# Kernel tuning notes

Hardware: AMD Instinct MI355X
Metric: run time of the kernel (lower is better)

## Reference

```python
import jax, jax.numpy as jnp
import numpy as np

B, L, LH, D, H = 32, 512, 2048, 1024, 4
DK = D // H  # dot-attn head dim
NEG = -1e9


def _ln(x, g, b, eps=1e-5):
    m = x.mean(-1, keepdims=True)
    v = ((x - m) ** 2).mean(-1, keepdims=True)
    return (x - m) / jnp.sqrt(v + eps) * g + b


def setup_inputs() -> dict:
    key = jax.random.key(0)
    ks = jax.random.split(key, 16)
    s = 0.05
    inp = {
        "seq_emb": jax.random.normal(ks[0], (B, L, D), jnp.float32),
        "seq_mask": jnp.ones((B, L), jnp.float32),
        "his_seq_emb": jax.random.normal(ks[1], (B, LH, D), jnp.float32),
        "his_seq_mask": jnp.ones((B, LH), jnp.float32),
        # dot-product MHA (bias=True)
        "sa_wq": jax.random.normal(ks[2], (D, D), jnp.float32) * s,
        "sa_bq": jnp.zeros((D,), jnp.float32),
        "sa_wk": jax.random.normal(ks[3], (D, D), jnp.float32) * s,
        "sa_bk": jnp.zeros((D,), jnp.float32),
        "sa_wv": jax.random.normal(ks[4], (D, D), jnp.float32) * s,
        "sa_bv": jnp.zeros((D,), jnp.float32),
        "sa_wo": jax.random.normal(ks[5], (D, D), jnp.float32) * s,
        "sa_bo": jnp.zeros((D,), jnp.float32),
        # short LayerNorm
        "sn_g": jnp.ones((D,), jnp.float32),
        "sn_b": jnp.zeros((D,), jnp.float32),
        # additive MHA (h=1, bias=False)
        "aa_wq": jax.random.normal(ks[6], (D, D), jnp.float32) * s,
        "aa_wk": jax.random.normal(ks[7], (D, D), jnp.float32) * s,
        "aa_wv": jax.random.normal(ks[8], (D, D), jnp.float32) * s,
        "aa_wo": jax.random.normal(ks[9], (D, D), jnp.float32) * s,
        "aa_wa": jax.random.normal(ks[10], (D,), jnp.float32) * s,
        # long LayerNorm
        "ln_g": jnp.ones((D,), jnp.float32),
        "ln_b": jnp.zeros((D,), jnp.float32),
    }
    return inp


def reference(seq_emb, seq_mask, his_seq_emb, his_seq_mask,
              sa_wq, sa_bq, sa_wk, sa_bk, sa_wv, sa_bv, sa_wo, sa_bo,
              sn_g, sn_b, aa_wq, aa_wk, aa_wv, aa_wo, aa_wa, ln_g, ln_b):
    # ---- dot-product self attention over seq_emb (dropout = eval/no-op) ----
    def split_heads(x):  # (B,L,D) -> (B,H,L,DK)
        return x.reshape(B, -1, H, DK).transpose(0, 2, 1, 3)

    q = split_heads(seq_emb @ sa_wq + sa_bq)
    k = split_heads(seq_emb @ sa_wk + sa_bk)
    v = split_heads(seq_emb @ sa_wv + sa_bv)
    scores = jnp.einsum('bhqd,bhkd->bhqk', q, k) / jnp.sqrt(jnp.float32(DK))
    scores = jnp.where(seq_mask[:, None, None, :] == 0, NEG, scores)
    p_attn = jax.nn.softmax(scores, axis=-1)  # (B,H,L,L)
    ctx = jnp.einsum('bhqk,bhkd->bhqd', p_attn, v)
    ctx = ctx.transpose(0, 2, 1, 3).reshape(B, L, D)
    sa_out = ctx @ sa_wo + sa_bo

    poi_attn = _ln(sa_out, sn_g, sn_b) * seq_mask[:, :, None]
    poi_hidden = poi_attn.mean(axis=1, keepdims=True)  # (B,1,D)

    # ---- additive (Bahdanau) attention, h=1, Lq=1 ----
    aq = poi_hidden @ aa_wq        # (B,1,D)
    ak = his_seq_emb @ aa_wk       # (B,LH,D)
    av = his_seq_emb @ aa_wv       # (B,LH,D)
    feats = jnp.tanh(aq[:, :, None, :] + ak[:, None, :, :])  # (B,1,LH,D)
    a_scores = jnp.einsum('bqkd,d->bqk', feats, aa_wa)        # (B,1,LH)
    a_scores = jnp.where(his_seq_mask[:, None, :] == 0, NEG, a_scores)
    a_w = jax.nn.softmax(a_scores, axis=-1)
    a_ctx = jnp.einsum('bqk,bkd->bqd', a_w, av)               # (B,1,D)
    aa_out = a_ctx @ aa_wo

    his_poi_hidden = poi_hidden + _ln(aa_out, ln_g, ln_b)     # (B,1,D)

    attn_weight = p_attn[:, 0, :, :]                          # (B,L,L)
    seq_hidden = jnp.concatenate([poi_hidden, his_poi_hidden], axis=-1)[:, 0, :]  # (B,2D)
    return seq_hidden, attn_weight
```

## Files before the change

kernel.cpp:

```cpp
#include <hip/hip_runtime.h>

#define NEGV (-1000000000.0f)

typedef __attribute__((ext_vector_type(8))) short sh8;
typedef __attribute__((ext_vector_type(4))) short sh4;
typedef __attribute__((ext_vector_type(8))) __bf16 bf16x8;
typedef __attribute__((ext_vector_type(4))) float f32x4;

__device__ __forceinline__ float b2f(unsigned short u) {
  unsigned v = ((unsigned)u) << 16;
  return __builtin_bit_cast(float, v);
}
__device__ __forceinline__ unsigned short f2b(float f) {
  unsigned x = __builtin_bit_cast(unsigned, f);
  unsigned r = (x + 0x7fffu + ((x >> 16) & 1u)) >> 16;
  return (unsigned short)r;
}
__device__ __forceinline__ void g2l16(const void* g, void* l) {
  __builtin_amdgcn_global_load_lds((const __attribute__((address_space(1))) unsigned int*)g,
                                   (__attribute__((address_space(3))) unsigned int*)l, 16, 0, 0);
}
__device__ __forceinline__ f32x4 mfma16(bf16x8 a, bf16x8 b, f32x4 c) {
  return __builtin_amdgcn_mfma_f32_16x16x32_bf16(a, b, c, 0, 0, 0);
}
__device__ __forceinline__ float fast_tanh(float x) {
  x = fminf(fmaxf(x, -15.f), 15.f);
  float e = __expf(2.f * x);
  return (e - 1.f) / (e + 1.f);
}

__global__ void cvt_all(const float* __restrict__ sa, unsigned short* __restrict__ da, int n4a,
                        const float* __restrict__ sb, unsigned short* __restrict__ db, int n4b)
{
  int stride = gridDim.x * blockDim.x;
  int i0 = blockIdx.x * blockDim.x + threadIdx.x;
  for (int i = i0; i < n4a; i += stride) {
    float4 v = ((const float4*)sa)[i];
    sh4 o;
    o[0] = (short)f2b(v.x); o[1] = (short)f2b(v.y);
    o[2] = (short)f2b(v.z); o[3] = (short)f2b(v.w);
    ((sh4*)da)[i] = o;
  }
  for (int i = i0; i < n4b; i += stride) {
    float4 v = ((const float4*)sb)[i];
    sh4 o;
    o[0] = (short)f2b(v.x); o[1] = (short)f2b(v.y);
    o[2] = (short)f2b(v.z); o[3] = (short)f2b(v.w);
    ((sh4*)db)[i] = o;
  }
}

__global__ void tcvt5(const float* __restrict__ s0, const float* __restrict__ s1,
                      const float* __restrict__ s2, const float* __restrict__ s3,
                      const float* __restrict__ s4,
                      unsigned short* __restrict__ d0, unsigned short* __restrict__ d1,
                      unsigned short* __restrict__ d2, unsigned short* __restrict__ d3,
                      unsigned short* __restrict__ d4)
{
  __shared__ float tile[64][65];
  const float* src; unsigned short* dst;
  switch (blockIdx.z) {
    case 0: src = s0; dst = d0; break;
    case 1: src = s1; dst = d1; break;
    case 2: src = s2; dst = d2; break;
    case 3: src = s3; dst = d3; break;
    default: src = s4; dst = d4; break;
  }
  int bx = blockIdx.x, by = blockIdx.y;
  int tx = threadIdx.x & 63, ty = threadIdx.x >> 6;
#pragma unroll
  for (int i = 0; i < 16; ++i) {
    int r = i * 4 + ty;
    tile[r][tx] = src[(size_t)(by * 64 + r) * 1024 + bx * 64 + tx];
  }
  __syncthreads();
#pragma unroll
  for (int i = 0; i < 16; ++i) {
    int r = i * 4 + ty;
    dst[(size_t)(bx * 64 + r) * 1024 + by * 64 + tx] = f2b(tile[tx][r]);
  }
}

template<int EPI>
__global__ __launch_bounds__(512, 1)
void gemm256(const unsigned short* __restrict__ A, const unsigned short* __restrict__ Bt,
             int nbx, int nby, int bxm,
             const float* __restrict__ b0, const float* __restrict__ b1,
             const float* __restrict__ b2,
             unsigned short* __restrict__ O0, unsigned short* __restrict__ O1,
             unsigned short* __restrict__ O2,
             const float* __restrict__ aq, const float* __restrict__ wa,
             float* __restrict__ sc)
{
  __shared__ char lds[131072];
  const int tid = threadIdx.x;
  const int w = tid >> 6, l = tid & 63;
  const int wm = w >> 2, wn = w & 3;
  const int lr = l & 15, g = l >> 4;

  const int wg = blockIdx.x;
  const int cpx = gridDim.x >> 3;
  const int wgid = (wg & 7) * cpx + (wg >> 3);
  int bx, by;
  if (bxm) { bx = wgid / nby; by = wgid - bx * nby; }
  else     { bx = wgid % nbx; by = wgid / nbx; }
  const size_t m0 = (size_t)by * 256;
  const int n0 = bx * 256;

  f32x4 acc[8][4] = {};
  bf16x8 fa[4], fb[4];

  const int srow = w * 8 + (l >> 3);
  const int schunk = ((l & 7) ^ ((l >> 3) & 7)) * 8;
  const unsigned short* gA = A + (m0 + srow) * 1024 + schunk;
  const unsigned short* gB = Bt + ((size_t)n0 + srow) * 1024 + schunk;
  const int ldst = w * 1024;

  const int chs = lr & 7;
  const int aRd0 = wm * 16384 + lr * 128;
  const int bRd0 = 32768 + (wn >> 1) * 16384 + (wn & 1) * 8192 + lr * 128;
  const int ck0 = ((0 * 4 + g) ^ chs) * 16;
  const int ck1 = ((1 * 4 + g) ^ chs) * 16;

#define STG_A(BUF, AH, RH, KK) \
  g2l16(gA + ((AH) * 128 + (RH) * 64) * 1024 + (KK), \
        lds + (BUF) * 65536 + (AH) * 16384 + (RH) * 8192 + ldst)
#define STG_B(BUF, BH, RH, KK) \
  g2l16(gB + ((BH) * 128 + (RH) * 64) * 1024 + (KK), \
        lds + (BUF) * 65536 + 32768 + (BH) * 16384 + (RH) * 8192 + ldst)

#define PH(BUFOFF, CK, IH, STAGES, TAIL)                                      \
  {                                                                           \
    const char* pb_ = lds + (BUFOFF);                                         \
    if ((IH) == 0) {                                                          \
      _Pragma("unroll") for (int j = 0; j < 4; ++j)                           \
        fb[j] = *(const bf16x8*)(pb_ + bRd0 + j * 2048 + (CK));               \
    }                                                                         \
    _Pragma("unroll") for (int i = 0; i < 4; ++i)                             \
      fa[i] = *(const bf16x8*)(pb_ + aRd0 + (IH) * 8192 + i * 2048 + (CK));   \
    STAGES;                                                                   \
    __builtin_amdgcn_sched_barrier(0);                                        \
    asm volatile("s_barrier" ::: "memory");                                   \
    asm volatile("s_waitcnt lgkmcnt(0)" ::: "memory");                        \
    __builtin_amdgcn_sched_barrier(0);                                        \
    __builtin_amdgcn_s_setprio(1);                                            \
    _Pragma("unroll") for (int i = 0; i < 4; ++i)                             \
      _Pragma("unroll") for (int j = 0; j < 4; ++j)                           \
        acc[(IH) * 4 + i][j] = mfma16(fa[i], fb[j], acc[(IH) * 4 + i][j]);    \
    __builtin_amdgcn_s_setprio(0);                                            \
    TAIL;                                                                     \
    asm volatile("s_barrier" ::: "memory");                                   \
  }

  STG_A(0, 0, 0, 0); STG_A(0, 0, 1, 0); STG_A(0, 1, 0, 0); STG_A(0, 1, 1, 0);
  STG_B(0, 0, 0, 0); STG_B(0, 0, 1, 0); STG_B(0, 1, 0, 0); STG_B(0, 1, 1, 0);
  STG_A(1, 0, 0, 64); STG_A(1, 1, 0, 64);
  asm volatile("s_waitcnt vmcnt(0)" ::: "memory");
  asm volatile("s_barrier" ::: "memory");

#pragma unroll 1
  for (int t = 0; t < 8; ++t) {
    const int k1 = (2 * t + 1) * 64, k2 = (2 * t + 2) * 64, k3 = (2 * t + 3) * 64;
    const bool st = (t < 7);
    PH(0,     ck0, 0, { STG_A(1, 0, 1, k1); STG_A(1, 1, 1, k1); }, {})
    PH(0,     ck0, 1, { STG_B(1, 0, 0, k1); STG_B(1, 0, 1, k1); }, {})
    PH(0,     ck1, 0, { STG_B(1, 1, 0, k1); STG_B(1, 1, 1, k1); }, {})
    PH(0,     ck1, 1, { if (st) { STG_A(0, 0, 0, k2); STG_A(0, 1, 0, k2); } },
       { if (st) { asm volatile("s_waitcnt vmcnt(2)" ::: "memory"); }
         else    { asm volatile("s_waitcnt vmcnt(0)" ::: "memory"); } })
    PH(65536, ck0, 0, { if (st) { STG_A(0, 0, 1, k2); STG_A(0, 1, 1, k2); } }, {})
    PH(65536, ck0, 1, { if (st) { STG_B(0, 0, 0, k2); STG_B(0, 0, 1, k2); } }, {})
    PH(65536, ck1, 0, { if (st) { STG_B(0, 1, 0, k2); STG_B(0, 1, 1, k2); } }, {})
    PH(65536, ck1, 1, { if (st) { STG_A(1, 0, 0, k3); STG_A(1, 1, 0, k3); } },
       { if (st) { asm volatile("s_waitcnt vmcnt(2)" ::: "memory"); } })
  }
#undef PH
#undef STG_A
#undef STG_B

  if (EPI == 0) {
#pragma unroll
    for (int j = 0; j < 4; ++j) {
      int col = n0 + wn * 64 + j * 16 + lr;
      float bv = b0[col];
#pragma unroll
      for (int i = 0; i < 8; ++i) {
        size_t rowb = m0 + wm * 128 + i * 16 + g * 4;
#pragma unroll
        for (int r = 0; r < 4; ++r)
          O0[(rowb + r) * 1024 + col] = f2b(acc[i][j][r] + bv);
      }
    }
  } else if (EPI == 1) {
#pragma unroll
    for (int j = 0; j < 4; ++j) {
      int col3 = n0 + wn * 64 + j * 16 + lr;
      int part = col3 >> 10, c = col3 & 1023;
      float bv = (part == 0) ? b0[c] : (part == 1) ? b1[c] : b2[c];
      if (part < 2) {
        unsigned short* O = part == 0 ? O0 : O1;
#pragma unroll
        for (int i = 0; i < 8; ++i) {
          size_t rowb = m0 + wm * 128 + i * 16 + g * 4;
#pragma unroll
          for (int r = 0; r < 4; ++r)
            O[(rowb + r) * 1024 + c] = f2b(acc[i][j][r] + bv);
        }
      } else {
        int h = c >> 8, d = c & 255;
#pragma unroll
        for (int i = 0; i < 8; ++i) {
          size_t row = m0 + wm * 128 + i * 16 + g * 4;
          int bb = (int)(row >> 9), ll = (int)(row & 511);
          size_t base = ((size_t)(bb * 4 + h) * 256 + d) * 512 + ll;
#pragma unroll
          for (int r = 0; r < 4; ++r)
            O2[base + r] = f2b(acc[i][j][r] + bv);
        }
      }
    }
  } else {
    const int bb = (int)(m0 >> 11);
#pragma unroll
    for (int i = 0; i < 8; ++i) {
      float rp[4] = {0.f, 0.f, 0.f, 0.f};
#pragma unroll
      for (int j = 0; j < 4; ++j) {
        int col = n0 + wn * 64 + j * 16 + lr;
        float wav = wa[col];
        float aqv = aq[bb * 1024 + col];
#pragma unroll
        for (int r = 0; r < 4; ++r)
          rp[r] += wav * fast_tanh(acc[i][j][r] + aqv);
      }
#pragma unroll
      for (int off = 1; off < 16; off <<= 1)
#pragma unroll
        for (int r = 0; r < 4; ++r)
          rp[r] += __shfl_xor(rp[r], off, 64);
      if (lr == 0) {
        size_t rowb = m0 + wm * 128 + i * 16 + g * 4;
#pragma unroll
        for (int r = 0; r < 4; ++r)
          atomicAdd(&sc[rowb + r], rp[r]);
      }
    }
  }
}

__global__ __launch_bounds__(256, 4)
void attn_kernel(const unsigned short* __restrict__ q, const unsigned short* __restrict__ k,
                 const unsigned short* __restrict__ vT, const float* __restrict__ seq_mask,
                 unsigned short* __restrict__ ctx, float* __restrict__ attn_out)
{
  __shared__ char smem[34304];
  unsigned short* Qs = (unsigned short*)smem;
  unsigned short* Ps = (unsigned short*)smem;
  float* redm = (float*)(smem + 33280);
  float* reds = (float*)(smem + 33792);
  const int t = threadIdx.x, w = t >> 6, l = t & 63;
  const int lr = l & 15, g = l >> 4, lk8 = g * 8;
  const int wg = blockIdx.x;
  const int wgid = (wg & 7) * 256 + (wg >> 3);
  const int qt = wgid & 15, bh = wgid >> 4;
  const int h = bh & 3, b = bh >> 2;
  const int l0 = qt * 32;

  for (int idx = t; idx < 32 * 32; idx += 256) {
    int r = idx >> 5, ch = (idx & 31) * 8;
    *(sh8*)&Qs[r * 264 + ch] =
        *(const sh8*)&q[((size_t)(b * 512 + l0 + r)) * 1024 + h * 256 + ch];
  }
  __syncthreads();

  f32x4 accs[2][8] = {};
  const unsigned short* kbase = k + ((size_t)b * 512) * 1024 + h * 256;
#pragma unroll
  for (int ds = 0; ds < 8; ++ds) {
    int d0 = ds * 32;
    bf16x8 a0 = *(const bf16x8*)&Qs[lr * 264 + d0 + lk8];
    bf16x8 a1 = *(const bf16x8*)&Qs[(16 + lr) * 264 + d0 + lk8];
#pragma unroll
    for (int j = 0; j < 8; ++j) {
      int kj = w * 128 + j * 16 + lr;
      bf16x8 bb = *(const bf16x8*)&kbase[(size_t)kj * 1024 + d0 + lk8];
      accs[0][j] = mfma16(a0, bb, accs[0][j]);
      accs[1][j] = mfma16(a1, bb, accs[1][j]);
    }
  }

#pragma unroll
  for (int j = 0; j < 8; ++j) {
    int col = w * 128 + j * 16 + lr;
    float mv = seq_mask[b * 512 + col];
    bool msk = (mv == 0.f);
#pragma unroll
    for (int i = 0; i < 2; ++i)
#pragma unroll
      for (int r = 0; r < 4; ++r)
        accs[i][j][r] = msk ? NEGV : accs[i][j][r] * 0.0625f;
  }

  float mx[2][4], sm[2][4];
#pragma unroll
  for (int i = 0; i < 2; ++i)
#pragma unroll
    for (int r = 0; r < 4; ++r) {
      float m = accs[i][0][r];
#pragma unroll
      for (int j = 1; j < 8; ++j) m = fmaxf(m, accs[i][j][r]);
      mx[i][r] = m;
    }
#pragma unroll
  for (int off = 1; off < 16; off <<= 1)
#pragma unroll
    for (int i = 0; i < 2; ++i)
#pragma unroll
      for (int r = 0; r < 4; ++r)
        mx[i][r] = fmaxf(mx[i][r], __shfl_xor(mx[i][r], off, 64));
  if (lr == 0) {
#pragma unroll
    for (int i = 0; i < 2; ++i)
#pragma unroll
      for (int r = 0; r < 4; ++r)
        redm[w * 32 + i * 16 + g * 4 + r] = mx[i][r];
  }
  __syncthreads();
#pragma unroll
  for (int i = 0; i < 2; ++i)
#pragma unroll
    for (int r = 0; r < 4; ++r) {
      int row = i * 16 + g * 4 + r;
      mx[i][r] = fmaxf(fmaxf(redm[row], redm[32 + row]),
                       fmaxf(redm[64 + row], redm[96 + row]));
      sm[i][r] = 0.f;
    }

#pragma unroll
  for (int i = 0; i < 2; ++i)
#pragma unroll
    for (int j = 0; j < 8; ++j)
#pragma unroll
      for (int r = 0; r < 4; ++r) {
        float p = __expf(accs[i][j][r] - mx[i][r]);
        accs[i][j][r] = p;
        sm[i][r] += p;
      }
#pragma unroll
  for (int off = 1; off < 16; off <<= 1)
#pragma unroll
    for (int i = 0; i < 2; ++i)
#pragma unroll
      for (int r = 0; r < 4; ++r)
        sm[i][r] += __shfl_xor(sm[i][r], off, 64);
  if (lr == 0) {
#pragma unroll
    for (int i = 0; i < 2; ++i)
#pragma unroll
      for (int r = 0; r < 4; ++r)
        reds[w * 32 + i * 16 + g * 4 + r] = sm[i][r];
  }
  __syncthreads();
#pragma unroll
  for (int i = 0; i < 2; ++i)
#pragma unroll
    for (int r = 0; r < 4; ++r) {
      int row = i * 16 + g * 4 + r;
      float s = reds[row] + reds[32 + row] + reds[64 + row] + reds[96 + row];
      sm[i][r] = 1.f / s;
    }

#pragma unroll
  for (int i = 0; i < 2; ++i)
#pragma unroll
    for (int j = 0; j < 8; ++j) {
      int col = w * 128 + j * 16 + lr;
#pragma unroll
      for (int r = 0; r < 4; ++r) {
        int row = i * 16 + g * 4 + r;
        float pn = accs[i][j][r] * sm[i][r];
        Ps[row * 520 + col] = f2b(pn);
        if (h == 0)
          attn_out[((size_t)(b * 512 + l0 + row)) * 512 + col] = pn;
      }
    }
  __syncthreads();

  f32x4 acco[2][4] = {};
  const unsigned short* vbase = vT + ((size_t)(b * 4 + h)) * 256 * 512;
#pragma unroll
  for (int ks = 0; ks < 16; ++ks) {
    int kj0 = ks * 32;
    bf16x8 a0 = *(const bf16x8*)&Ps[lr * 520 + kj0 + lk8];
    bf16x8 a1 = *(const bf16x8*)&Ps[(16 + lr) * 520 + kj0 + lk8];
#pragma unroll
    for (int j = 0; j < 4; ++j) {
      int d = w * 64 + j * 16 + lr;
      bf16x8 bb = *(const bf16x8*)&vbase[(size_t)d * 512 + kj0 + lk8];
      acco[0][j] = mfma16(a0, bb, acco[0][j]);
      acco[1][j] = mfma16(a1, bb, acco[1][j]);
    }
  }
#pragma unroll
  for (int i = 0; i < 2; ++i)
#pragma unroll
    for (int j = 0; j < 4; ++j) {
      int col = w * 64 + j * 16 + lr;
#pragma unroll
      for (int r = 0; r < 4; ++r) {
        int row = i * 16 + g * 4 + r;
        ctx[((size_t)(b * 512 + l0 + row)) * 1024 + h * 256 + col] = f2b(acco[i][j][r]);
      }
    }
}

__global__ __launch_bounds__(256)
void ln_mean(const unsigned short* __restrict__ sa, const float* __restrict__ g,
             const float* __restrict__ bt, const float* __restrict__ mask,
             float* __restrict__ poi_sum)
{
  const int b = blockIdx.y, ch = blockIdx.x;
  const int t = threadIdx.x, w = t >> 6, l = t & 63;
  float gg[16], bb[16];
#pragma unroll
  for (int j = 0; j < 16; ++j) { gg[j] = g[l * 16 + j]; bb[j] = bt[l * 16 + j]; }
  float accv[16];
#pragma unroll
  for (int j = 0; j < 16; ++j) accv[j] = 0.f;
  for (int rr = 0; rr < 16; ++rr) {
    int row = ch * 64 + w * 16 + rr;
    const unsigned short* rp = sa + ((size_t)(b * 512 + row)) * 1024 + l * 16;
    float x[16];
    sh8 v0 = *(const sh8*)rp;
    sh8 v1 = *(const sh8*)(rp + 8);
#pragma unroll
    for (int j = 0; j < 8; ++j) {
      x[j] = b2f((unsigned short)v0[j]);
      x[8 + j] = b2f((unsigned short)v1[j]);
    }
    float s = 0.f, s2 = 0.f;
#pragma unroll
    for (int j = 0; j < 16; ++j) { s += x[j]; s2 += x[j] * x[j]; }
#pragma unroll
    for (int off = 1; off < 64; off <<= 1) {
      s += __shfl_xor(s, off, 64);
      s2 += __shfl_xor(s2, off, 64);
    }
    float mean = s * (1.f / 1024.f);
    float var = s2 * (1.f / 1024.f) - mean * mean;
    float rinv = rsqrtf(var + 1e-5f);
    float mk = mask[b * 512 + row];
#pragma unroll
    for (int j = 0; j < 16; ++j) accv[j] += ((x[j] - mean) * rinv * gg[j] + bb[j]) * mk;
  }
#pragma unroll
  for (int j = 0; j < 16; ++j) atomicAdd(&poi_sum[b * 1024 + l * 16 + j], accv[j]);
}

__global__ void finalize_poi(const float* __restrict__ ps, float* __restrict__ poi) {
  int i = blockIdx.x * 256 + threadIdx.x;
  if (i < 32 * 1024) poi[i] = ps[i] * (1.f / 512.f);
}

__global__ __launch_bounds__(256)
void gemv32(const float* __restrict__ in, const float* __restrict__ W, float* __restrict__ out)
{
  const int b = blockIdx.y;
  const int n = blockIdx.x * 256 + threadIdx.x;
  const float* ib = in + b * 1024;
  float acc = 0.f;
  for (int d = 0; d < 1024; d += 4) {
    acc += ib[d]     * W[(size_t)d * 1024 + n]
         + ib[d + 1] * W[(size_t)(d + 1) * 1024 + n]
         + ib[d + 2] * W[(size_t)(d + 2) * 1024 + n]
         + ib[d + 3] * W[(size_t)(d + 3) * 1024 + n];
  }
  out[b * 1024 + n] = acc;
}

__global__ __launch_bounds__(256)
void softmax_his(float* __restrict__ sc, const float* __restrict__ mask)
{
  __shared__ float red[4];
  const int b = blockIdx.x, t = threadIdx.x, w = t >> 6, l = t & 63;
  float v[8];
  float mx = -3.0e38f;
#pragma unroll
  for (int i = 0; i < 8; ++i) {
    int kk = t + i * 256;
    float s = (mask[b * 2048 + kk] == 0.f) ? NEGV : sc[b * 2048 + kk];
    v[i] = s;
    mx = fmaxf(mx, s);
  }
#pragma unroll
  for (int off = 1; off < 64; off <<= 1) mx = fmaxf(mx, __shfl_xor(mx, off, 64));
  if (l == 0) red[w] = mx;
  __syncthreads();
  mx = fmaxf(fmaxf(red[0], red[1]), fmaxf(red[2], red[3]));
  float sum = 0.f;
#pragma unroll
  for (int i = 0; i < 8; ++i) { v[i] = __expf(v[i] - mx); sum += v[i]; }
#pragma unroll
  for (int off = 1; off < 64; off <<= 1) sum += __shfl_xor(sum, off, 64);
  __syncthreads();
  if (l == 0) red[w] = sum;
  __syncthreads();
  sum = red[0] + red[1] + red[2] + red[3];
  float inv = 1.f / sum;
#pragma unroll
  for (int i = 0; i < 8; ++i) sc[b * 2048 + t + i * 256] = v[i] * inv;
}

__global__ __launch_bounds__(256)
void hw_kernel(const float* __restrict__ aw, const unsigned short* __restrict__ his,
               float* __restrict__ hw)
{
  const int b = blockIdx.y, kc = blockIdx.x, t = threadIdx.x;
  const int cb = t * 4;
  float a0 = 0.f, a1 = 0.f, a2 = 0.f, a3 = 0.f;
  for (int kk = 0; kk < 256; ++kk) {
    int k = kc * 256 + kk;
    float wg = aw[b * 2048 + k];
    sh4 vv = *(const sh4*)&his[((size_t)(b * 2048 + k)) * 1024 + cb];
    a0 += wg * b2f((unsigned short)vv[0]);
    a1 += wg * b2f((unsigned short)vv[1]);
    a2 += wg * b2f((unsigned short)vv[2]);
    a3 += wg * b2f((unsigned short)vv[3]);
  }
  atomicAdd(&hw[b * 1024 + cb + 0], a0);
  atomicAdd(&hw[b * 1024 + cb + 1], a1);
  atomicAdd(&hw[b * 1024 + cb + 2], a2);
  atomicAdd(&hw[b * 1024 + cb + 3], a3);
}

__global__ __launch_bounds__(256)
void final_kernel(const float* __restrict__ aa_out, const float* __restrict__ g,
                  const float* __restrict__ bt, const float* __restrict__ poi,
                  float* __restrict__ out)
{
  __shared__ float r1[4], r2[4];
  const int b = blockIdx.x, t = threadIdx.x, w = t >> 6, l = t & 63;
  float x[4];
#pragma unroll
  for (int j = 0; j < 4; ++j) x[j] = aa_out[b * 1024 + t * 4 + j];
  float s = 0.f, s2 = 0.f;
#pragma unroll
  for (int j = 0; j < 4; ++j) { s += x[j]; s2 += x[j] * x[j]; }
#pragma unroll
  for (int off = 1; off < 64; off <<= 1) {
    s += __shfl_xor(s, off, 64);
    s2 += __shfl_xor(s2, off, 64);
  }
  if (l == 0) { r1[w] = s; r2[w] = s2; }
  __syncthreads();
  s = r1[0] + r1[1] + r1[2] + r1[3];
  s2 = r2[0] + r2[1] + r2[2] + r2[3];
  float mean = s * (1.f / 1024.f);
  float var = s2 * (1.f / 1024.f) - mean * mean;
  float rinv = rsqrtf(var + 1e-5f);
#pragma unroll
  for (int j = 0; j < 4; ++j) {
    int c = t * 4 + j;
    float lnv = (x[j] - mean) * rinv * g[c] + bt[c];
    float pv = poi[b * 1024 + c];
    out[b * 2048 + c] = pv;
    out[b * 2048 + 1024 + c] = pv + lnv;
  }
}

extern "C" void kernel_launch(void* const* d_in, const int* in_sizes, int n_in,
                              void* d_out, int out_size, void* d_ws, size_t ws_size,
                              hipStream_t stream)
{
  const float* seq_emb  = (const float*)d_in[0];
  const float* seq_mask = (const float*)d_in[1];
  const float* his_emb  = (const float*)d_in[2];
  const float* his_mask = (const float*)d_in[3];
  const float* sa_wq = (const float*)d_in[4];
  const float* sa_bq = (const float*)d_in[5];
  const float* sa_wk = (const float*)d_in[6];
  const float* sa_bk = (const float*)d_in[7];
  const float* sa_wv = (const float*)d_in[8];
  const float* sa_bv = (const float*)d_in[9];
  const float* sa_wo = (const float*)d_in[10];
  const float* sa_bo = (const float*)d_in[11];
  const float* sn_g  = (const float*)d_in[12];
  const float* sn_b  = (const float*)d_in[13];
  const float* aa_wq = (const float*)d_in[14];
  const float* aa_wk = (const float*)d_in[15];
  const float* aa_wv = (const float*)d_in[16];
  const float* aa_wo = (const float*)d_in[17];
  const float* aa_wa = (const float*)d_in[18];
  const float* ln_g  = (const float*)d_in[19];
  const float* ln_b  = (const float*)d_in[20];
  float* out = (float*)d_out;

  char* p = (char*)d_ws;
  size_t off = 0;
  auto alloc = [&](size_t bytes) -> void* {
    void* r = p + off;
    off += (bytes + 255) & ~(size_t)255;
    return r;
  };
  unsigned short* seqb = (unsigned short*)alloc((size_t)16384 * 1024 * 2);
  unsigned short* hisb = (unsigned short*)alloc((size_t)65536 * 1024 * 2);
  unsigned short* wcat = (unsigned short*)alloc((size_t)3072 * 1024 * 2);
  unsigned short* woT  = (unsigned short*)alloc((size_t)1024 * 1024 * 2);
  unsigned short* awkT = (unsigned short*)alloc((size_t)1024 * 1024 * 2);
  unsigned short* qb   = (unsigned short*)alloc((size_t)16384 * 1024 * 2);
  unsigned short* kb   = (unsigned short*)alloc((size_t)16384 * 1024 * 2);
  unsigned short* vTb  = (unsigned short*)alloc((size_t)16384 * 1024 * 2);
  unsigned short* ctxb = (unsigned short*)alloc((size_t)16384 * 1024 * 2);
  unsigned short* saob = (unsigned short*)alloc((size_t)16384 * 1024 * 2);
  float* poi_sum = (float*)alloc((size_t)32 * 1024 * 4);
  float* poi     = (float*)alloc((size_t)32 * 1024 * 4);
  float* aqb     = (float*)alloc((size_t)32 * 1024 * 4);
  float* ascore  = (float*)alloc((size_t)32 * 2048 * 4);
  float* hwb     = (float*)alloc((size_t)32 * 1024 * 4);
  float* actx    = (float*)alloc((size_t)32 * 1024 * 4);
  float* aaout   = (float*)alloc((size_t)32 * 1024 * 4);
  if (off > ws_size) return;

  hipMemsetAsync(poi_sum, 0, (size_t)32 * 1024 * 4, stream);
  hipMemsetAsync(ascore, 0, (size_t)32 * 2048 * 4, stream);
  hipMemsetAsync(hwb, 0, (size_t)32 * 1024 * 4, stream);

  cvt_all<<<2048, 256, 0, stream>>>(seq_emb, seqb, 16384 * 1024 / 4,
                                    his_emb, hisb, 65536 * 1024 / 4);
  tcvt5<<<dim3(16, 16, 5), 256, 0, stream>>>(
      sa_wq, sa_wk, sa_wv, sa_wo, aa_wk,
      wcat, wcat + (size_t)1024 * 1024, wcat + (size_t)2048 * 1024, woT, awkT);

  gemm256<1><<<768, 512, 0, stream>>>(seqb, wcat, 12, 64, 1, sa_bq, sa_bk, sa_bv,
                                      qb, kb, vTb, nullptr, nullptr, nullptr);

  attn_kernel<<<2048, 256, 0, stream>>>(qb, kb, vTb, seq_mask, ctxb, out + 65536);

  gemm256<0><<<256, 512, 0, stream>>>(ctxb, woT, 4, 64, 0, sa_bo, nullptr, nullptr,
                                      saob, nullptr, nullptr, nullptr, nullptr, nullptr);
  ln_mean<<<dim3(8, 32), 256, 0, stream>>>(saob, sn_g, sn_b, seq_mask, poi_sum);
  finalize_poi<<<128, 256, 0, stream>>>(poi_sum, poi);
  gemv32<<<dim3(4, 32), 256, 0, stream>>>(poi, aa_wq, aqb);

  gemm256<2><<<1024, 512, 0, stream>>>(hisb, awkT, 4, 256, 0, nullptr, nullptr, nullptr,
                                       nullptr, nullptr, nullptr, aqb, aa_wa, ascore);
  softmax_his<<<32, 256, 0, stream>>>(ascore, his_mask);
  hw_kernel<<<dim3(8, 32), 256, 0, stream>>>(ascore, hisb, hwb);
  gemv32<<<dim3(4, 32), 256, 0, stream>>>(hwb, aa_wv, actx);
  gemv32<<<dim3(4, 32), 256, 0, stream>>>(actx, aa_wo, aaout);
  final_kernel<<<32, 256, 0, stream>>>(aaout, ln_g, ln_b, poi, out);
}
```

Measured before the change: 788.4 us.

## Replace 256x256 pipelined GEMM with simple 128x128 tile kernel and fuse poi finalize into gemv

Replaces the hand-pipelined 256x256-tile, 512-thread GEMM that uses 128KB of double-buffered LDS with a 128x128-tile, 256-thread kernel. The new kernel has a 32-wide K step, a single small LDS buffer, two __syncthreads per step and no prefetch overlap, and it launches more blocks with up to four per CU. The poi finalize kernel is also merged into the aa_wq gemv, which scales by 1/512 after the dot product, saving one launch. The simpler GEMM gives up the global-load/MFMA overlap and halves data reuse per tile, so it risks exposing memory latency.

```diff
diff --git a/kernel.cpp b/kernel.cpp
--- a/kernel.cpp
+++ b/kernel.cpp
@@ -82,9 +82,9 @@
 }
 
 template<int EPI>
-__global__ __launch_bounds__(512, 1)
-void gemm256(const unsigned short* __restrict__ A, const unsigned short* __restrict__ Bt,
-             int nbx, int nby, int bxm,
+__global__ __launch_bounds__(256, 4)
+void gemm128(const unsigned short* __restrict__ A, const unsigned short* __restrict__ Bt,
+             int nbx,
              const float* __restrict__ b0, const float* __restrict__ b1,
              const float* __restrict__ b2,
              unsigned short* __restrict__ O0, unsigned short* __restrict__ O1,
@@ -92,100 +92,66 @@
              const float* __restrict__ aq, const float* __restrict__ wa,
              float* __restrict__ sc)
 {
-  __shared__ char lds[131072];
+  __shared__ unsigned short ldsA[4096];
+  __shared__ unsigned short ldsB[4096];
   const int tid = threadIdx.x;
   const int w = tid >> 6, l = tid & 63;
-  const int wm = w >> 2, wn = w & 3;
+  const int wr = w >> 1, wc = w & 1;
   const int lr = l & 15, g = l >> 4;
 
   const int wg = blockIdx.x;
   const int cpx = gridDim.x >> 3;
   const int wgid = (wg & 7) * cpx + (wg >> 3);
-  int bx, by;
-  if (bxm) { bx = wgid / nby; by = wgid - bx * nby; }
-  else     { bx = wgid % nbx; by = wgid / nbx; }
-  const size_t m0 = (size_t)by * 256;
-  const int n0 = bx * 256;
-
-  f32x4 acc[8][4] = {};
-  bf16x8 fa[4], fb[4];
-
-  const int srow = w * 8 + (l >> 3);
-  const int schunk = ((l & 7) ^ ((l >> 3) & 7)) * 8;
-  const unsigned short* gA = A + (m0 + srow) * 1024 + schunk;
-  const unsigned short* gB = Bt + ((size_t)n0 + srow) * 1024 + schunk;
-  const int ldst = w * 1024;
-
-  const int chs = lr & 7;
-  const int aRd0 = wm * 16384 + lr * 128;
-  const int bRd0 = 32768 + (wn >> 1) * 16384 + (wn & 1) * 8192 + lr * 128;
-  const int ck0 = ((0 * 4 + g) ^ chs) * 16;
-  const int ck1 = ((1 * 4 + g) ^ chs) * 16;
-
-#define STG_A(BUF, AH, RH, KK) \
-  g2l16(gA + ((AH) * 128 + (RH) * 64) * 1024 + (KK), \
-        lds + (BUF) * 65536 + (AH) * 16384 + (RH) * 8192 + ldst)
-#define STG_B(BUF, BH, RH, KK) \
-  g2l16(gB + ((BH) * 128 + (RH) * 64) * 1024 + (KK), \
-        lds + (BUF) * 65536 + 32768 + (BH) * 16384 + (RH) * 8192 + ldst)
-
-#define PH(BUFOFF, CK, IH, STAGES, TAIL)                                      \
-  {                                                                           \
-    const char* pb_ = lds + (BUFOFF);                                         \
-    if ((IH) == 0) {                                                          \
-      _Pragma("unroll") for (int j = 0; j < 4; ++j)                           \
-        fb[j] = *(const bf16x8*)(pb_ + bRd0 + j * 2048 + (CK));               \
-    }                                                                         \
-    _Pragma("unroll") for (int i = 0; i < 4; ++i)                             \
-      fa[i] = *(const bf16x8*)(pb_ + aRd0 + (IH) * 8192 + i * 2048 + (CK));   \
-    STAGES;                                                                   \
-    __builtin_amdgcn_sched_barrier(0);                                        \
-    asm volatile("s_barrier" ::: "memory");                                   \
-    asm volatile("s_waitcnt lgkmcnt(0)" ::: "memory");                        \
-    __builtin_amdgcn_sched_barrier(0);                                        \
-    __builtin_amdgcn_s_setprio(1);                                            \
-    _Pragma("unroll") for (int i = 0; i < 4; ++i)                             \
-      _Pragma("unroll") for (int j = 0; j < 4; ++j)                           \
-        acc[(IH) * 4 + i][j] = mfma16(fa[i], fb[j], acc[(IH) * 4 + i][j]);    \
-    __builtin_amdgcn_s_setprio(0);                                            \
-    TAIL;                                                                     \
-    asm volatile("s_barrier" ::: "memory");                                   \
-  }
-
-  STG_A(0, 0, 0, 0); STG_A(0, 0, 1, 0); STG_A(0, 1, 0, 0); STG_A(0, 1, 1, 0);
-  STG_B(0, 0, 0, 0); STG_B(0, 0, 1, 0); STG_B(0, 1, 0, 0); STG_B(0, 1, 1, 0);
-  STG_A(1, 0, 0, 64); STG_A(1, 1, 0, 64);
-  asm volatile("s_waitcnt vmcnt(0)" ::: "memory");
-  asm volatile("s_barrier" ::: "memory");
+  const int bx = wgid % nbx, by = wgid / nbx;
+  const size_t m0 = (size_t)by * 128;
+  const int n0 = bx * 128;
+
+  f32x4 acc[4][4] = {};
+
+  const int srow = tid >> 2;
+  const int sk = ((tid & 3) ^ ((tid >> 2) & 3)) * 8;
+  const unsigned short* gA = A + (m0 + srow) * 1024 + sk;
+  const unsigned short* gB = Bt + ((size_t)n0 + srow) * 1024 + sk;
+  char* const dA0 = (char*)ldsA + w * 1024;
+  char* const dA1 = (char*)ldsA + 4096 + w * 1024;
+  char* const dB0 = (char*)ldsB + w * 1024;
+  char* const dB1 = (char*)ldsB + 4096 + w * 1024;
+
+  const int cswz = (g ^ (lr & 3)) * 16;
+  const int aoff = (wr * 64 + lr) * 64 + cswz;
+  const int boff = (wc * 64 + lr) * 64 + cswz;
 
 #pragma unroll 1
-  for (int t = 0; t < 8; ++t) {
-    const int k1 = (2 * t + 1) * 64, k2 = (2 * t + 2) * 64, k3 = (2 * t + 3) * 64;
-    const bool st = (t < 7);
-    PH(0,     ck0, 0, { STG_A(1, 0, 1, k1); STG_A(1, 1, 1, k1); }, {})
-    PH(0,     ck0, 1, { STG_B(1, 0, 0, k1); STG_B(1, 0, 1, k1); }, {})
-    PH(0,     ck1, 0, { STG_B(1, 1, 0, k1); STG_B(1, 1, 1, k1); }, {})
-    PH(0,     ck1, 1, { if (st) { STG_A(0, 0, 0, k2); STG_A(0, 1, 0, k2); } },
-       { if (st) { asm volatile("s_waitcnt vmcnt(2)" ::: "memory"); }
-         else    { asm volatile("s_waitcnt vmcnt(0)" ::: "memory"); } })
-    PH(65536, ck0, 0, { if (st) { STG_A(0, 0, 1, k2); STG_A(0, 1, 1, k2); } }, {})
-    PH(65536, ck0, 1, { if (st) { STG_B(0, 0, 0, k2); STG_B(0, 0, 1, k2); } }, {})
-    PH(65536, ck1, 0, { if (st) { STG_B(0, 1, 0, k2); STG_B(0, 1, 1, k2); } }, {})
-    PH(65536, ck1, 1, { if (st) { STG_A(1, 0, 0, k3); STG_A(1, 1, 0, k3); } },
-       { if (st) { asm volatile("s_waitcnt vmcnt(2)" ::: "memory"); } })
-  }
-#undef PH
-#undef STG_A
-#undef STG_B
+  for (int kt = 0; kt < 32; ++kt) {
+    const int k0 = kt * 32;
+    g2l16(gA + k0, dA0);
+    g2l16(gA + 64 * 1024 + k0, dA1);
+    g2l16(gB + k0, dB0);
+    g2l16(gB + 64 * 1024 + k0, dB1);
+    __syncthreads();
+    bf16x8 af[4], bf[4];
+#pragma unroll
+    for (int i = 0; i < 4; ++i)
+      af[i] = *(const bf16x8*)((const char*)ldsA + aoff + i * 1024);
+#pragma unroll
+    for (int j = 0; j < 4; ++j)
+      bf[j] = *(const bf16x8*)((const char*)ldsB + boff + j * 1024);
+#pragma unroll
+    for (int i = 0; i < 4; ++i)
+#pragma unroll
+      for (int j = 0; j < 4; ++j)
+        acc[i][j] = mfma16(af[i], bf[j], acc[i][j]);
+    __syncthreads();
+  }
 
   if (EPI == 0) {
 #pragma unroll
     for (int j = 0; j < 4; ++j) {
-      int col = n0 + wn * 64 + j * 16 + lr;
+      int col = n0 + wc * 64 + j * 16 + lr;
       float bv = b0[col];
 #pragma unroll
-      for (int i = 0; i < 8; ++i) {
-        size_t rowb = m0 + wm * 128 + i * 16 + g * 4;
+      for (int i = 0; i < 4; ++i) {
+        size_t rowb = m0 + wr * 64 + i * 16 + g * 4;
 #pragma unroll
         for (int r = 0; r < 4; ++r)
           O0[(rowb + r) * 1024 + col] = f2b(acc[i][j][r] + bv);
@@ -194,14 +160,14 @@
   } else if (EPI == 1) {
 #pragma unroll
     for (int j = 0; j < 4; ++j) {
-      int col3 = n0 + wn * 64 + j * 16 + lr;
+      int col3 = n0 + wc * 64 + j * 16 + lr;
       int part = col3 >> 10, c = col3 & 1023;
       float bv = (part == 0) ? b0[c] : (part == 1) ? b1[c] : b2[c];
       if (part < 2) {
         unsigned short* O = part == 0 ? O0 : O1;
 #pragma unroll
-        for (int i = 0; i < 8; ++i) {
-          size_t rowb = m0 + wm * 128 + i * 16 + g * 4;
+        for (int i = 0; i < 4; ++i) {
+          size_t rowb = m0 + wr * 64 + i * 16 + g * 4;
 #pragma unroll
           for (int r = 0; r < 4; ++r)
             O[(rowb + r) * 1024 + c] = f2b(acc[i][j][r] + bv);
@@ -209,8 +175,8 @@
       } else {
         int h = c >> 8, d = c & 255;
 #pragma unroll
-        for (int i = 0; i < 8; ++i) {
-          size_t row = m0 + wm * 128 + i * 16 + g * 4;
+        for (int i = 0; i < 4; ++i) {
+          size_t row = m0 + wr * 64 + i * 16 + g * 4;
           int bb = (int)(row >> 9), ll = (int)(row & 511);
           size_t base = ((size_t)(bb * 4 + h) * 256 + d) * 512 + ll;
 #pragma unroll
@@ -222,11 +188,11 @@
   } else {
     const int bb = (int)(m0 >> 11);
 #pragma unroll
-    for (int i = 0; i < 8; ++i) {
+    for (int i = 0; i < 4; ++i) {
       float rp[4] = {0.f, 0.f, 0.f, 0.f};
 #pragma unroll
       for (int j = 0; j < 4; ++j) {
-        int col = n0 + wn * 64 + j * 16 + lr;
+        int col = n0 + wc * 64 + j * 16 + lr;
         float wav = wa[col];
         float aqv = aq[bb * 1024 + col];
 #pragma unroll
@@ -239,7 +205,7 @@
         for (int r = 0; r < 4; ++r)
           rp[r] += __shfl_xor(rp[r], off, 64);
       if (lr == 0) {
-        size_t rowb = m0 + wm * 128 + i * 16 + g * 4;
+        size_t rowb = m0 + wr * 64 + i * 16 + g * 4;
 #pragma unroll
         for (int r = 0; r < 4; ++r)
           atomicAdd(&sc[rowb + r], rp[r]);
@@ -457,9 +423,22 @@
   for (int j = 0; j < 16; ++j) atomicAdd(&poi_sum[b * 1024 + l * 16 + j], accv[j]);
 }
 
-__global__ void finalize_poi(const float* __restrict__ ps, float* __restrict__ poi) {
-  int i = blockIdx.x * 256 + threadIdx.x;
-  if (i < 32 * 1024) poi[i] = ps[i] * (1.f / 512.f);
+__global__ __launch_bounds__(256)
+void poi_gemv(const float* __restrict__ ps, const float* __restrict__ wq,
+              float* __restrict__ poi, float* __restrict__ aq)
+{
+  const int b = blockIdx.y;
+  const int n = blockIdx.x * 256 + threadIdx.x;
+  const float* ib = ps + b * 1024;
+  float acc = 0.f;
+  for (int d = 0; d < 1024; d += 4) {
+    acc += ib[d]     * wq[(size_t)d * 1024 + n]
+         + ib[d + 1] * wq[(size_t)(d + 1) * 1024 + n]
+         + ib[d + 2] * wq[(size_t)(d + 2) * 1024 + n]
+         + ib[d + 3] * wq[(size_t)(d + 3) * 1024 + n];
+  }
+  poi[b * 1024 + n] = ib[n] * (1.f / 512.f);
+  aq[b * 1024 + n] = acc * (1.f / 512.f);
 }
 
 __global__ __launch_bounds__(256)
@@ -631,18 +610,17 @@
       sa_wq, sa_wk, sa_wv, sa_wo, aa_wk,
       wcat, wcat + (size_t)1024 * 1024, wcat + (size_t)2048 * 1024, woT, awkT);
 
-  gemm256<1><<<768, 512, 0, stream>>>(seqb, wcat, 12, 64, 1, sa_bq, sa_bk, sa_bv,
-                                      qb, kb, vTb, nullptr, nullptr, nullptr);
+  gemm128<1><<<3072, 256, 0, stream>>>(seqb, wcat, 24, sa_bq, sa_bk, sa_bv,
+                                       qb, kb, vTb, nullptr, nullptr, nullptr);
 
   attn_kernel<<<2048, 256, 0, stream>>>(qb, kb, vTb, seq_mask, ctxb, out + 65536);
 
-  gemm256<0><<<256, 512, 0, stream>>>(ctxb, woT, 4, 64, 0, sa_bo, nullptr, nullptr,
-                                      saob, nullptr, nullptr, nullptr, nullptr, nullptr);
+  gemm128<0><<<1024, 256, 0, stream>>>(ctxb, woT, 8, sa_bo, nullptr, nullptr,
+                                       saob, nullptr, nullptr, nullptr, nullptr, nullptr);
   ln_mean<<<dim3(8, 32), 256, 0, stream>>>(saob, sn_g, sn_b, seq_mask, poi_sum);
-  finalize_poi<<<128, 256, 0, stream>>>(poi_sum, poi);
-  gemv32<<<dim3(4, 32), 256, 0, stream>>>(poi, aa_wq, aqb);
-
-  gemm256<2><<<1024, 512, 0, stream>>>(hisb, awkT, 4, 256, 0, nullptr, nullptr, nullptr,
+  poi_gemv<<<dim3(4, 32), 256, 0, stream>>>(poi_sum, aa_wq, poi, aqb);
+
+  gemm128<2><<<4096, 256, 0, stream>>>(hisb, awkT, 8, nullptr, nullptr, nullptr,
                                        nullptr, nullptr, nullptr, aqb, aa_wa, ascore);
   softmax_his<<<32, 256, 0, stream>>>(ascore, his_mask);
   hw_kernel<<<dim3(8, 32), 256, 0, stream>>>(ascore, hisb, hwb);
```

Result: slower. 815.2 us (+3.4%).

## Fuse prep, poi and softmax kernels; retile additive-attention key GEMM to 128x128

Applied to the files above, without the earlier changes.

Merges the fp32-to-bf16 conversion and weight-transpose kernels into one launch. Merges the poi finalize step into the aa_wq GEMV, and merges the softmax into the history-weighting kernel. The three memsets become one contiguous memset, which assumes the buffers are allocated back to back. The tanh-score GEMM over the history sequence moves from a 256x256 one-block-per-CU tile to a 128x128 tile with 4 waves and up to 4 blocks per CU, aiming for better occupancy and load balance. Each softhw block now recomputes the full softmax redundantly, and the smaller tile gives less data reuse per block.

```diff
diff --git a/kernel.cpp b/kernel.cpp
--- a/kernel.cpp
+++ b/kernel.cpp
@@ -29,45 +29,48 @@
   return (e - 1.f) / (e + 1.f);
 }
 
-__global__ void cvt_all(const float* __restrict__ sa, unsigned short* __restrict__ da, int n4a,
-                        const float* __restrict__ sb, unsigned short* __restrict__ db, int n4b)
-{
-  int stride = gridDim.x * blockDim.x;
-  int i0 = blockIdx.x * blockDim.x + threadIdx.x;
-  for (int i = i0; i < n4a; i += stride) {
-    float4 v = ((const float4*)sa)[i];
-    sh4 o;
-    o[0] = (short)f2b(v.x); o[1] = (short)f2b(v.y);
-    o[2] = (short)f2b(v.z); o[3] = (short)f2b(v.w);
-    ((sh4*)da)[i] = o;
-  }
-  for (int i = i0; i < n4b; i += stride) {
-    float4 v = ((const float4*)sb)[i];
-    sh4 o;
-    o[0] = (short)f2b(v.x); o[1] = (short)f2b(v.y);
-    o[2] = (short)f2b(v.z); o[3] = (short)f2b(v.w);
-    ((sh4*)db)[i] = o;
-  }
-}
-
-__global__ void tcvt5(const float* __restrict__ s0, const float* __restrict__ s1,
-                      const float* __restrict__ s2, const float* __restrict__ s3,
-                      const float* __restrict__ s4,
-                      unsigned short* __restrict__ d0, unsigned short* __restrict__ d1,
-                      unsigned short* __restrict__ d2, unsigned short* __restrict__ d3,
-                      unsigned short* __restrict__ d4)
-{
+__global__ __launch_bounds__(256)
+void prep(const float* __restrict__ seq, unsigned short* __restrict__ seqb, int n4a,
+          const float* __restrict__ his, unsigned short* __restrict__ hisb, int n4b,
+          const float* __restrict__ s0, const float* __restrict__ s1,
+          const float* __restrict__ s2, const float* __restrict__ s3,
+          const float* __restrict__ s4,
+          unsigned short* __restrict__ d0, unsigned short* __restrict__ d1,
+          unsigned short* __restrict__ d2, unsigned short* __restrict__ d3,
+          unsigned short* __restrict__ d4)
+{
+  const int t = threadIdx.x;
+  if (blockIdx.x < 2048) {
+    const int stride = 2048 * 256;
+    for (int i = blockIdx.x * 256 + t; i < n4a; i += stride) {
+      float4 v = ((const float4*)seq)[i];
+      sh4 o;
+      o[0] = (short)f2b(v.x); o[1] = (short)f2b(v.y);
+      o[2] = (short)f2b(v.z); o[3] = (short)f2b(v.w);
+      ((sh4*)seqb)[i] = o;
+    }
+    for (int i = blockIdx.x * 256 + t; i < n4b; i += stride) {
+      float4 v = ((const float4*)his)[i];
+      sh4 o;
+      o[0] = (short)f2b(v.x); o[1] = (short)f2b(v.y);
+      o[2] = (short)f2b(v.z); o[3] = (short)f2b(v.w);
+      ((sh4*)hisb)[i] = o;
+    }
+    return;
+  }
   __shared__ float tile[64][65];
+  int z2 = blockIdx.x - 2048;
+  int zz = z2 >> 8, rem = z2 & 255;
+  int by = rem >> 4, bx = rem & 15;
   const float* src; unsigned short* dst;
-  switch (blockIdx.z) {
+  switch (zz) {
     case 0: src = s0; dst = d0; break;
     case 1: src = s1; dst = d1; break;
     case 2: src = s2; dst = d2; break;
     case 3: src = s3; dst = d3; break;
     default: src = s4; dst = d4; break;
   }
-  int bx = blockIdx.x, by = blockIdx.y;
-  int tx = threadIdx.x & 63, ty = threadIdx.x >> 6;
+  int tx = t & 63, ty = t >> 6;
 #pragma unroll
   for (int i = 0; i < 16; ++i) {
     int r = i * 4 + ty;
@@ -88,9 +91,7 @@
              const float* __restrict__ b0, const float* __restrict__ b1,
              const float* __restrict__ b2,
              unsigned short* __restrict__ O0, unsigned short* __restrict__ O1,
-             unsigned short* __restrict__ O2,
-             const float* __restrict__ aq, const float* __restrict__ wa,
-             float* __restrict__ sc)
+             unsigned short* __restrict__ O2)
 {
   __shared__ char lds[131072];
   const int tid = threadIdx.x;
@@ -191,7 +192,7 @@
           O0[(rowb + r) * 1024 + col] = f2b(acc[i][j][r] + bv);
       }
     }
-  } else if (EPI == 1) {
+  } else {
 #pragma unroll
     for (int j = 0; j < 4; ++j) {
       int col3 = n0 + wn * 64 + j * 16 + lr;
@@ -219,31 +220,109 @@
         }
       }
     }
-  } else {
-    const int bb = (int)(m0 >> 11);
-#pragma unroll
-    for (int i = 0; i < 8; ++i) {
-      float rp[4] = {0.f, 0.f, 0.f, 0.f};
-#pragma unroll
-      for (int j = 0; j < 4; ++j) {
-        int col = n0 + wn * 64 + j * 16 + lr;
-        float wav = wa[col];
-        float aqv = aq[bb * 1024 + col];
-#pragma unroll
-        for (int r = 0; r < 4; ++r)
-          rp[r] += wav * fast_tanh(acc[i][j][r] + aqv);
-      }
-#pragma unroll
-      for (int off = 1; off < 16; off <<= 1)
-#pragma unroll
-        for (int r = 0; r < 4; ++r)
-          rp[r] += __shfl_xor(rp[r], off, 64);
-      if (lr == 0) {
-        size_t rowb = m0 + wm * 128 + i * 16 + g * 4;
-#pragma unroll
-        for (int r = 0; r < 4; ++r)
-          atomicAdd(&sc[rowb + r], rp[r]);
-      }
+  }
+}
+
+__global__ __launch_bounds__(256, 4)
+void gemm128b64(const unsigned short* __restrict__ A, const unsigned short* __restrict__ Bt,
+                int nbx,
+                const float* __restrict__ aq, const float* __restrict__ wa,
+                float* __restrict__ sc)
+{
+  __shared__ unsigned short ldsA[8192];
+  __shared__ unsigned short ldsB[8192];
+  const int tid = threadIdx.x;
+  const int w = tid >> 6, l = tid & 63;
+  const int wr = w >> 1, wc = w & 1;
+  const int lr = l & 15, g = l >> 4;
+
+  const int wg = blockIdx.x;
+  const int cpx = gridDim.x >> 3;
+  const int wgid = (wg & 7) * cpx + (wg >> 3);
+  const int bx = wgid % nbx, by = wgid / nbx;
+  const size_t m0 = (size_t)by * 128;
+  const int n0 = bx * 128;
+
+  f32x4 acc[4][4] = {};
+
+  const int srow = tid >> 3;
+  const int sk = ((tid & 7) ^ ((tid >> 3) & 7)) * 8;
+  const unsigned short* gA = A + (m0 + srow) * 1024 + sk;
+  const unsigned short* gB = Bt + ((size_t)n0 + srow) * 1024 + sk;
+  const int ldst = w * 1024;
+
+  const int chs = lr & 7;
+  const int ck0 = ((0 * 4 + g) ^ chs) * 16;
+  const int ck1 = ((1 * 4 + g) ^ chs) * 16;
+  const int aRd = (wr * 64 + lr) * 128;
+  const int bRd = (wc * 64 + lr) * 128;
+
+#define STG64(KT)                                                        \
+  { const int ko_ = (KT) * 64;                                           \
+    g2l16(gA + ko_,             (char*)ldsA + ldst);                     \
+    g2l16(gA + 32 * 1024 + ko_, (char*)ldsA + 4096 + ldst);              \
+    g2l16(gA + 64 * 1024 + ko_, (char*)ldsA + 8192 + ldst);              \
+    g2l16(gA + 96 * 1024 + ko_, (char*)ldsA + 12288 + ldst);             \
+    g2l16(gB + ko_,             (char*)ldsB + ldst);                     \
+    g2l16(gB + 32 * 1024 + ko_, (char*)ldsB + 4096 + ldst);              \
+    g2l16(gB + 64 * 1024 + ko_, (char*)ldsB + 8192 + ldst);              \
+    g2l16(gB + 96 * 1024 + ko_, (char*)ldsB + 12288 + ldst); }
+
+  STG64(0)
+#pragma unroll 1
+  for (int kt = 0; kt < 16; ++kt) {
+    __syncthreads();
+    bf16x8 af[4], bf[4];
+#pragma unroll
+    for (int i = 0; i < 4; ++i)
+      af[i] = *(const bf16x8*)((const char*)ldsA + aRd + i * 2048 + ck0);
+#pragma unroll
+    for (int j = 0; j < 4; ++j)
+      bf[j] = *(const bf16x8*)((const char*)ldsB + bRd + j * 2048 + ck0);
+#pragma unroll
+    for (int i = 0; i < 4; ++i)
+#pragma unroll
+      for (int j = 0; j < 4; ++j)
+        acc[i][j] = mfma16(af[i], bf[j], acc[i][j]);
+#pragma unroll
+    for (int i = 0; i < 4; ++i)
+      af[i] = *(const bf16x8*)((const char*)ldsA + aRd + i * 2048 + ck1);
+#pragma unroll
+    for (int j = 0; j < 4; ++j)
+      bf[j] = *(const bf16x8*)((const char*)ldsB + bRd + j * 2048 + ck1);
+#pragma unroll
+    for (int i = 0; i < 4; ++i)
+#pragma unroll
+      for (int j = 0; j < 4; ++j)
+        acc[i][j] = mfma16(af[i], bf[j], acc[i][j]);
+    __syncthreads();
+    if (kt < 15) STG64(kt + 1)
+  }
+#undef STG64
+
+  const int bb = (int)(m0 >> 11);
+#pragma unroll
+  for (int i = 0; i < 4; ++i) {
+    float rp[4] = {0.f, 0.f, 0.f, 0.f};
+#pragma unroll
+    for (int j = 0; j < 4; ++j) {
+      int col = n0 + wc * 64 + j * 16 + lr;
+      float wav = wa[col];
+      float aqv = aq[bb * 1024 + col];
+#pragma unroll
+      for (int r = 0; r < 4; ++r)
+        rp[r] += wav * fast_tanh(acc[i][j][r] + aqv);
+    }
+#pragma unroll
+    for (int off = 1; off < 16; off <<= 1)
+#pragma unroll
+      for (int r = 0; r < 4; ++r)
+        rp[r] += __shfl_xor(rp[r], off, 64);
+    if (lr == 0) {
+      size_t rowb = m0 + wr * 64 + i * 16 + g * 4;
+#pragma unroll
+      for (int r = 0; r < 4; ++r)
+        atomicAdd(&sc[rowb + r], rp[r]);
     }
   }
 }
@@ -457,9 +536,76 @@
   for (int j = 0; j < 16; ++j) atomicAdd(&poi_sum[b * 1024 + l * 16 + j], accv[j]);
 }
 
-__global__ void finalize_poi(const float* __restrict__ ps, float* __restrict__ poi) {
-  int i = blockIdx.x * 256 + threadIdx.x;
-  if (i < 32 * 1024) poi[i] = ps[i] * (1.f / 512.f);
+__global__ __launch_bounds__(256)
+void poi_gemv(const float* __restrict__ ps, const float* __restrict__ wq,
+              float* __restrict__ poi, float* __restrict__ aq)
+{
+  const int b = blockIdx.y;
+  const int n = blockIdx.x * 256 + threadIdx.x;
+  const float* ib = ps + b * 1024;
+  float acc = 0.f;
+  for (int d = 0; d < 1024; d += 4) {
+    acc += ib[d]     * wq[(size_t)d * 1024 + n]
+         + ib[d + 1] * wq[(size_t)(d + 1) * 1024 + n]
+         + ib[d + 2] * wq[(size_t)(d + 2) * 1024 + n]
+         + ib[d + 3] * wq[(size_t)(d + 3) * 1024 + n];
+  }
+  poi[b * 1024 + n] = ib[n] * (1.f / 512.f);
+  aq[b * 1024 + n] = acc * (1.f / 512.f);
+}
+
+__global__ __launch_bounds__(256)
+void softhw(const float* __restrict__ sc, const float* __restrict__ mask,
+            const unsigned short* __restrict__ his, float* __restrict__ hw)
+{
+  __shared__ float wloc[2048];
+  __shared__ float red[4];
+  const int b = blockIdx.y, kc = blockIdx.x;
+  const int t = threadIdx.x, w = t >> 6, l = t & 63;
+  float v[8];
+  float mx = -3.0e38f;
+#pragma unroll
+  for (int i = 0; i < 8; ++i) {
+    int kk = t + i * 256;
+    float s = (mask[b * 2048 + kk] == 0.f) ? NEGV : sc[b * 2048 + kk];
+    v[i] = s;
+    mx = fmaxf(mx, s);
+  }
+#pragma unroll
+  for (int off = 1; off < 64; off <<= 1) mx = fmaxf(mx, __shfl_xor(mx, off, 64));
+  if (l == 0) red[w] = mx;
+  __syncthreads();
+  mx = fmaxf(fmaxf(red[0], red[1]), fmaxf(red[2], red[3]));
+  float sum = 0.f;
+#pragma unroll
+  for (int i = 0; i < 8; ++i) {
+    v[i] = __expf(v[i] - mx);
+    wloc[t + i * 256] = v[i];
+    sum += v[i];
+  }
+#pragma unroll
+  for (int off = 1; off < 64; off <<= 1) sum += __shfl_xor(sum, off, 64);
+  __syncthreads();
+  if (l == 0) red[w] = sum;
+  __syncthreads();
+  sum = red[0] + red[1] + red[2] + red[3];
+  const float inv = 1.f / sum;
+
+  const int cb = t * 4;
+  float a0 = 0.f, a1 = 0.f, a2 = 0.f, a3 = 0.f;
+  for (int kk = 0; kk < 256; ++kk) {
+    int k = kc * 256 + kk;
+    float wg = wloc[k] * inv;
+    sh4 vv = *(const sh4*)&his[((size_t)(b * 2048 + k)) * 1024 + cb];
+    a0 += wg * b2f((unsigned short)vv[0]);
+    a1 += wg * b2f((unsigned short)vv[1]);
+    a2 += wg * b2f((unsigned short)vv[2]);
+    a3 += wg * b2f((unsigned short)vv[3]);
+  }
+  atomicAdd(&hw[b * 1024 + cb + 0], a0);
+  atomicAdd(&hw[b * 1024 + cb + 1], a1);
+  atomicAdd(&hw[b * 1024 + cb + 2], a2);
+  atomicAdd(&hw[b * 1024 + cb + 3], a3);
 }
 
 __global__ __launch_bounds__(256)
@@ -476,61 +622,6 @@
          + ib[d + 3] * W[(size_t)(d + 3) * 1024 + n];
   }
   out[b * 1024 + n] = acc;
-}
-
-__global__ __launch_bounds__(256)
-void softmax_his(float* __restrict__ sc, const float* __restrict__ mask)
-{
-  __shared__ float red[4];
-  const int b = blockIdx.x, t = threadIdx.x, w = t >> 6, l = t & 63;
-  float v[8];
-  float mx = -3.0e38f;
-#pragma unroll
-  for (int i = 0; i < 8; ++i) {
-    int kk = t + i * 256;
-    float s = (mask[b * 2048 + kk] == 0.f) ? NEGV : sc[b * 2048 + kk];
-    v[i] = s;
-    mx = fmaxf(mx, s);
-  }
-#pragma unroll
-  for (int off = 1; off < 64; off <<= 1) mx = fmaxf(mx, __shfl_xor(mx, off, 64));
-  if (l == 0) red[w] = mx;
-  __syncthreads();
-  mx = fmaxf(fmaxf(red[0], red[1]), fmaxf(red[2], red[3]));
-  float sum = 0.f;
-#pragma unroll
-  for (int i = 0; i < 8; ++i) { v[i] = __expf(v[i] - mx); sum += v[i]; }
-#pragma unroll
-  for (int off = 1; off < 64; off <<= 1) sum += __shfl_xor(sum, off, 64);
-  __syncthreads();
-  if (l == 0) red[w] = sum;
-  __syncthreads();
-  sum = red[0] + red[1] + red[2] + red[3];
-  float inv = 1.f / sum;
-#pragma unroll
-  for (int i = 0; i < 8; ++i) sc[b * 2048 + t + i * 256] = v[i] * inv;
-}
-
-__global__ __launch_bounds__(256)
-void hw_kernel(const float* __restrict__ aw, const unsigned short* __restrict__ his,
-               float* __restrict__ hw)
-{
-  const int b = blockIdx.y, kc = blockIdx.x, t = threadIdx.x;
-  const int cb = t * 4;
-  float a0 = 0.f, a1 = 0.f, a2 = 0.f, a3 = 0.f;
-  for (int kk = 0; kk < 256; ++kk) {
-    int k = kc * 256 + kk;
-    float wg = aw[b * 2048 + k];
-    sh4 vv = *(const sh4*)&his[((size_t)(b * 2048 + k)) * 1024 + cb];
-    a0 += wg * b2f((unsigned short)vv[0]);
-    a1 += wg * b2f((unsigned short)vv[1]);
-    a2 += wg * b2f((unsigned short)vv[2]);
-    a3 += wg * b2f((unsigned short)vv[3]);
-  }
-  atomicAdd(&hw[b * 1024 + cb + 0], a0);
-  atomicAdd(&hw[b * 1024 + cb + 1], a1);
-  atomicAdd(&hw[b * 1024 + cb + 2], a2);
-  atomicAdd(&hw[b * 1024 + cb + 3], a3);
 }
 
 __global__ __launch_bounds__(256)
@@ -621,31 +712,26 @@
   float* aaout   = (float*)alloc((size_t)32 * 1024 * 4);
   if (off > ws_size) return;
 
-  hipMemsetAsync(poi_sum, 0, (size_t)32 * 1024 * 4, stream);
-  hipMemsetAsync(ascore, 0, (size_t)32 * 2048 * 4, stream);
-  hipMemsetAsync(hwb, 0, (size_t)32 * 1024 * 4, stream);
-
-  cvt_all<<<2048, 256, 0, stream>>>(seq_emb, seqb, 16384 * 1024 / 4,
-                                    his_emb, hisb, 65536 * 1024 / 4);
-  tcvt5<<<dim3(16, 16, 5), 256, 0, stream>>>(
-      sa_wq, sa_wk, sa_wv, sa_wo, aa_wk,
-      wcat, wcat + (size_t)1024 * 1024, wcat + (size_t)2048 * 1024, woT, awkT);
+  hipMemsetAsync(poi_sum, 0, (size_t)(6 * 32 * 1024) * 4, stream);
+
+  prep<<<3328, 256, 0, stream>>>(seq_emb, seqb, 16384 * 1024 / 4,
+                                 his_emb, hisb, 65536 * 1024 / 4,
+                                 sa_wq, sa_wk, sa_wv, sa_wo, aa_wk,
+                                 wcat, wcat + (size_t)1024 * 1024,
+                                 wcat + (size_t)2048 * 1024, woT, awkT);
 
   gemm256<1><<<768, 512, 0, stream>>>(seqb, wcat, 12, 64, 1, sa_bq, sa_bk, sa_bv,
-                                      qb, kb, vTb, nullptr, nullptr, nullptr);
+                                      qb, kb, vTb);
 
   attn_kernel<<<2048, 256, 0, stream>>>(qb, kb, vTb, seq_mask, ctxb, out + 65536);
 
   gemm256<0><<<256, 512, 0, stream>>>(ctxb, woT, 4, 64, 0, sa_bo, nullptr, nullptr,
-                                      saob, nullptr, nullptr, nullptr, nullptr, nullptr);
+                                      saob, nullptr, nullptr);
   ln_mean<<<dim3(8, 32), 256, 0, stream>>>(saob, sn_g, sn_b, seq_mask, poi_sum);
-  finalize_poi<<<128, 256, 0, stream>>>(poi_sum, poi);
-  gemv32<<<dim3(4, 32), 256, 0, stream>>>(poi, aa_wq, aqb);
-
-  gemm256<2><<<1024, 512, 0, stream>>>(hisb, awkT, 4, 256, 0, nullptr, nullptr, nullptr,
-                                       nullptr, nullptr, nullptr, aqb, aa_wa, ascore);
-  softmax_his<<<32, 256, 0, stream>>>(ascore, his_mask);
-  hw_kernel<<<dim3(8, 32), 256, 0, stream>>>(ascore, hisb, hwb);
+  poi_gemv<<<dim3(4, 32), 256, 0, stream>>>(poi_sum, aa_wq, poi, aqb);
+
+  gemm128b64<<<4096, 256, 0, stream>>>(hisb, awkT, 8, aqb, aa_wa, ascore);
+  softhw<<<dim3(8, 32), 256, 0, stream>>>(ascore, his_mask, hisb, hwb);
   gemv32<<<dim3(4, 32), 256, 0, stream>>>(hwb, aa_wv, actx);
   gemv32<<<dim3(4, 32), 256, 0, stream>>>(actx, aa_wo, aaout);
   final_kernel<<<32, 256, 0, stream>>>(aaout, ln_g, ln_b, poi, out);
```

Result: no change. 788.8 us (+0.1%).
